# Kernel optimization log

Measured on AMD Instinct MI355X. Metric: run time of the kernel, lower is better.

## Reference

```python
import math
import jax, jax.numpy as jnp
import numpy as np


def setup_inputs() -> dict:
    key = jax.random.key(0)
    k1, k2, k3, k4 = jax.random.split(key, 4)
    B, CK, CV, T, H, W = 4, 64, 512, 8, 30, 30
    mk = jax.random.normal(k1, (B, CK, T, H, W), dtype=jnp.float32)
    qk = jax.random.normal(k2, (B, CK, H, W), dtype=jnp.float32)
    mv = jax.random.normal(k3, (B, CV, T, H, W), dtype=jnp.float32)
    qv = jax.random.normal(k4, (B, CV, H, W), dtype=jnp.float32)
    return {"mk": mk, "qk": qk, "mv": mv, "qv": qv}


def reference(mk, qk, mv, qv):
    # mk: [B, CK, T, H, W], qk: [B, CK, H, W]
    # mv: [B, CV, T, H, W], qv: [B, CV, H, W]
    B, CK, T, H, W = mk.shape
    CV = mv.shape[1]
    mkf = mk.reshape(B, CK, T * H * W)          # [B, CK, THW]
    qkf = qk.reshape(B, CK, H * W)              # [B, CK, HW]
    # distance-based affinity: (2 a.b - |a|^2) / sqrt(CK)
    a_sq = jnp.sum(mkf * mkf, axis=1)[:, :, None]        # [B, THW, 1]
    ab = jnp.einsum('bcm,bcq->bmq', mkf, qkf)            # [B, THW, HW]
    affinity = (2.0 * ab - a_sq) * (1.0 / math.sqrt(CK))
    # softmax over the memory dimension (THW)
    affinity = jax.nn.softmax(affinity, axis=1)          # [B, THW, HW]
    # value readout
    mvf = mv.reshape(B, CV, T * H * W)                   # [B, CV, THW]
    mem = jnp.einsum('bcm,bmq->bcq', mvf, affinity)      # [B, CV, HW]
    mem = mem.reshape(B, CV, H, W)
    return jnp.concatenate([mem, qv], axis=1)            # [B, 2*CV, H, W]
```

## Files before the change

kernel.cpp:

```cpp
#include <hip/hip_runtime.h>

#define B_ 4
#define CK 64
#define CV 512
#define HW_ 900
#define THW 7200
#define MT 96
#define QB 64
#define CVB 128
#define NS 3
#define MSPL (THW / NS)
#define NIT (MSPL / MT)
#define MVP (MT + 8)
#define MKP (CK + 8)

typedef __attribute__((ext_vector_type(4))) float f32x4;
typedef __attribute__((ext_vector_type(4))) float float4_;
typedef __attribute__((ext_vector_type(8))) short s16x8;
typedef __attribute__((ext_vector_type(4))) short s16x4;

__device__ __forceinline__ short f2bf(float f) {
  union { float f; unsigned u; } x; x.f = f;
  unsigned u = x.u;
  return (short)((u + 0x7fffu + ((u >> 16) & 1u)) >> 16);
}

#define NBLK_A 113
#define NBLK_B 900
#define NBLK_C 14400
#define NBLK_D 1800
__global__ __launch_bounds__(256) void prep_kernel(const float* __restrict__ mk,
                                                   const float* __restrict__ qk,
                                                   const float* __restrict__ mv,
                                                   const float* __restrict__ qv,
                                                   short* __restrict__ mkT,
                                                   short* __restrict__ qkb,
                                                   short* __restrict__ mvb,
                                                   float* __restrict__ asq,
                                                   float* __restrict__ out) {
  int bid = blockIdx.x;
  if (bid < NBLK_A) {
    int idx = bid * 256 + threadIdx.x;
    if (idx >= B_ * THW) return;
    int b = idx / THW, m = idx - b * THW;
    const float* src = mk + (size_t)b * CK * THW + m;
    short row[CK];
    float acc = 0.f;
#pragma unroll
    for (int k = 0; k < CK; ++k) {
      float v = src[(size_t)k * THW];
      acc += v * v;
      row[k] = f2bf(v);
    }
    short* dst = mkT + (size_t)idx * CK;
#pragma unroll
    for (int c = 0; c < CK / 8; ++c)
      *reinterpret_cast<s16x8*>(dst + c * 8) = *reinterpret_cast<s16x8*>(row + c * 8);
    asq[idx] = acc * 0.18033688011112042f;
  } else if (bid < NBLK_A + NBLK_B) {
    int i = (bid - NBLK_A) * 256 + threadIdx.x;
    if (i < B_ * CK * HW_) qkb[i] = f2bf(qk[i] * 0.36067376022224085f);
  } else if (bid < NBLK_A + NBLK_B + NBLK_C) {
    int i = (bid - (NBLK_A + NBLK_B)) * 256 + threadIdx.x;
    float4_ v = reinterpret_cast<const float4_*>(mv)[i];
    s16x4 o;
    o[0] = f2bf(v[0]); o[1] = f2bf(v[1]); o[2] = f2bf(v[2]); o[3] = f2bf(v[3]);
    *reinterpret_cast<s16x4*>(mvb + (size_t)i * 4) = o;
  } else {
    int i = (bid - (NBLK_A + NBLK_B + NBLK_C)) * 256 + threadIdx.x;
    const int perb = CV * HW_ / 4;
    int b = i / perb, r = i - b * perb;
    float4_ v = reinterpret_cast<const float4_*>(qv)[i];
    *reinterpret_cast<float4_*>(out + (size_t)b * 2 * CV * HW_ + CV * HW_ + (size_t)r * 4) = v;
  }
}

__global__ __launch_bounds__(256, 3) void attn_kernel(const short* __restrict__ mkT,
                                                      const short* __restrict__ qkb,
                                                      const short* __restrict__ mvb,
                                                      const float* __restrict__ asq,
                                                      float* __restrict__ part,
                                                      float* __restrict__ denomp) {
  __shared__ short mv_t[CVB][MVP];
  __shared__ short mk_t[MT][MKP];
  __shared__ short e_t[4][16][MVP];
  __shared__ float asq_t[MT];

  const int tid = threadIdx.x;
  const int wave = tid >> 6, lane = tid & 63;
  const int g = lane >> 4, c = lane & 15;
  const int qb = blockIdx.x;
  const int cvc = blockIdx.y & 3, s = blockIdx.y >> 2;
  const int b = blockIdx.z;
  const int q = qb * QB + wave * 16 + c;
  const int cv0 = cvc * CVB;

  s16x8 qf[2];
  {
    const short* qs = qkb + (size_t)b * CK * HW_;
#pragma unroll
    for (int ks = 0; ks < 2; ++ks)
#pragma unroll
      for (int j = 0; j < 8; ++j)
        qf[ks][j] = (q < HW_) ? qs[(size_t)(ks * 32 + g * 8 + j) * HW_ + q] : (short)0;
  }

  f32x4 acc[8];
#pragma unroll
  for (int i = 0; i < 8; ++i) acc[i] = (f32x4){0.f, 0.f, 0.f, 0.f};
  float denom = 0.f;

  const short* mksrc = mkT + (size_t)b * THW * CK;
  const short* mvsrc = mvb + ((size_t)b * CV + cv0) * THW;
  const float* asrc = asq + (size_t)b * THW;

  for (int it = 0; it < NIT; ++it) {
    const int m0 = s * MSPL + it * MT;
    {
      const short* s0 = mksrc + (size_t)m0 * CK;
#pragma unroll
      for (int p = 0; p < 3; ++p) {
        int ch = tid + p * 256;
        int r = ch >> 3, c8 = (ch & 7) * 8;
        *reinterpret_cast<s16x8*>(&mk_t[r][c8]) =
            *reinterpret_cast<const s16x8*>(s0 + r * CK + c8);
      }
#pragma unroll
      for (int p = 0; p < 6; ++p) {
        int ch = tid + p * 256;
        int r = ch / 12, c8 = (ch % 12) * 8;
        *reinterpret_cast<s16x8*>(&mv_t[r][c8]) =
            *reinterpret_cast<const s16x8*>(mvsrc + (size_t)r * THW + m0 + c8);
      }
      if (tid < MT) asq_t[tid] = asrc[m0 + tid];
    }
    __syncthreads();

#pragma unroll
    for (int mf = 0; mf < 6; ++mf) {
      f32x4 sa = (f32x4){0.f, 0.f, 0.f, 0.f};
#pragma unroll
      for (int ks = 0; ks < 2; ++ks) {
        s16x8 a = *reinterpret_cast<const s16x8*>(&mk_t[mf * 16 + c][ks * 32 + g * 8]);
        sa = __builtin_amdgcn_mfma_f32_16x16x32_bf16(a, qf[ks], sa, 0, 0, 0);
      }
      const int mb = mf * 16 + g * 4;
      s16x4 e4;
#pragma unroll
      for (int r = 0; r < 4; ++r) {
        float e = exp2f(sa[r] - asq_t[mb + r]);
        denom += e;
        e4[r] = f2bf(e);
      }
      *reinterpret_cast<s16x4*>(&e_t[wave][c][mb]) = e4;
    }

#pragma unroll
    for (int ks = 0; ks < 3; ++ks) {
      s16x8 bfr = *reinterpret_cast<const s16x8*>(&e_t[wave][c][ks * 32 + g * 8]);
#pragma unroll
      for (int cf = 0; cf < 8; ++cf) {
        s16x8 afr = *reinterpret_cast<const s16x8*>(&mv_t[cf * 16 + c][ks * 32 + g * 8]);
        acc[cf] = __builtin_amdgcn_mfma_f32_16x16x32_bf16(afr, bfr, acc[cf], 0, 0, 0);
      }
    }
    __syncthreads();
  }

  denom += __shfl_xor(denom, 16);
  denom += __shfl_xor(denom, 32);
  if (cvc == 0 && lane < 16)
    denomp[((size_t)s * B_ + b) * 960 + qb * QB + wave * 16 + lane] = denom;

  float* pb = part + (size_t)(((s * B_ + b) * 4 + cvc) * 15 + qb) * 8192 + wave * 16 + c;
#pragma unroll
  for (int cf = 0; cf < 8; ++cf)
#pragma unroll
    for (int r = 0; r < 4; ++r)
      pb[(size_t)(cf * 16 + g * 4 + r) * 64] = acc[cf][r];
}

__global__ __launch_bounds__(256) void finalize_kernel(const float* __restrict__ part,
                                                       const float* __restrict__ denomp,
                                                       float* __restrict__ out) {
  int t = blockIdx.x * 256 + threadIdx.x;
  int q4 = t & 15;
  int cvl = (t >> 4) & 127;
  int r1 = t >> 11;
  int qb = r1 % 15;
  int r2 = r1 / 15;
  int cvc = r2 & 3;
  int b = r2 >> 2;
  int q0 = qb * QB + q4 * 4;
  if (q0 >= HW_) return;
  const size_t sstr = (size_t)B_ * 4 * 15 * 8192;
  size_t base = (size_t)((b * 4 + cvc) * 15 + qb) * 8192 + cvl * 64 + q4 * 4;
  f32x4 p = *reinterpret_cast<const f32x4*>(part + base);
  f32x4 p1 = *reinterpret_cast<const f32x4*>(part + base + sstr);
  f32x4 p2 = *reinterpret_cast<const f32x4*>(part + base + 2 * sstr);
  p = p + p1 + p2;
  const float* dp = denomp + (size_t)b * 960 + q0;
  f32x4 d = *reinterpret_cast<const f32x4*>(dp) +
            *reinterpret_cast<const f32x4*>(dp + B_ * 960) +
            *reinterpret_cast<const f32x4*>(dp + 2 * B_ * 960);
  f32x4 o;
#pragma unroll
  for (int j = 0; j < 4; ++j) o[j] = p[j] / d[j];
  *reinterpret_cast<f32x4*>(out + (size_t)b * 2 * CV * HW_ +
                            (size_t)(cvc * CVB + cvl) * HW_ + q0) = o;
}

extern "C" void kernel_launch(void* const* d_in, const int* in_sizes, int n_in,
                              void* d_out, int out_size, void* d_ws, size_t ws_size,
                              hipStream_t stream) {
  const float* mk = (const float*)d_in[0];
  const float* qk = (const float*)d_in[1];
  const float* mv = (const float*)d_in[2];
  const float* qv = (const float*)d_in[3];
  float* out = (float*)d_out;

  char* ws = (char*)d_ws;
  short* mvb   = (short*)ws;
  short* mkT   = (short*)(ws + 29491200);
  short* qkb   = (short*)(ws + 33177600);
  float* asq   = (float*)(ws + 33638400);
  float* denomp= (float*)(ws + 33753600);
  float* part  = (float*)(ws + 33799680);

  prep_kernel<<<dim3(NBLK_A + NBLK_B + NBLK_C + NBLK_D), dim3(256), 0, stream>>>(
      mk, qk, mv, qv, mkT, qkb, mvb, asq, out);
  attn_kernel<<<dim3(15, 4 * NS, B_), dim3(256), 0, stream>>>(mkT, qkb, mvb, asq, part, denomp);
  finalize_kernel<<<dim3(1920), dim3(256), 0, stream>>>(part, denomp, out);
}
```

Baseline: 237.2 us.

## Load mk/mv fragments directly from global and share exp tile across waves

Removes the LDS staging of the mk and mv tiles. Each wave now reads its mk and mv MFMA fragments straight from global memory, and only the exp (affinity) tile goes through shared memory. The work is repartitioned so each wave owns 32 value channels across all 64 queries instead of 16 queries across all 128 channels. The change also truncates instead of rounding when converting to bf16 and raises the occupancy hint to 4 blocks. In exchange it relies on L1/L2 for the repeated mk reads, since every wave now loads the same mk rows, and it adds a small precision loss from truncation.

```diff
diff --git a/kernel.cpp b/kernel.cpp
--- a/kernel.cpp
+++ b/kernel.cpp
@@ -11,8 +11,7 @@
 #define NS 3
 #define MSPL (THW / NS)
 #define NIT (MSPL / MT)
-#define MVP (MT + 8)
-#define MKP (CK + 8)
+#define ETP 104
 
 typedef __attribute__((ext_vector_type(4))) float f32x4;
 typedef __attribute__((ext_vector_type(4))) float float4_;
@@ -75,16 +74,13 @@
   }
 }
 
-__global__ __launch_bounds__(256, 3) void attn_kernel(const short* __restrict__ mkT,
+__global__ __launch_bounds__(256, 4) void attn_kernel(const short* __restrict__ mkT,
                                                       const short* __restrict__ qkb,
                                                       const short* __restrict__ mvb,
                                                       const float* __restrict__ asq,
                                                       float* __restrict__ part,
                                                       float* __restrict__ denomp) {
-  __shared__ short mv_t[CVB][MVP];
-  __shared__ short mk_t[MT][MKP];
-  __shared__ short e_t[4][16][MVP];
-  __shared__ float asq_t[MT];
+  __shared__ short e_t[64][ETP];
 
   const int tid = threadIdx.x;
   const int wave = tid >> 6, lane = tid & 63;
@@ -93,76 +89,73 @@
   const int cvc = blockIdx.y & 3, s = blockIdx.y >> 2;
   const int b = blockIdx.z;
   const int q = qb * QB + wave * 16 + c;
-  const int cv0 = cvc * CVB;
-
-  s16x8 qf[2];
+
+  s16x8 qkf[2];
   {
     const short* qs = qkb + (size_t)b * CK * HW_;
 #pragma unroll
     for (int ks = 0; ks < 2; ++ks)
 #pragma unroll
       for (int j = 0; j < 8; ++j)
-        qf[ks][j] = (q < HW_) ? qs[(size_t)(ks * 32 + g * 8 + j) * HW_ + q] : (short)0;
+        qkf[ks][j] = (q < HW_) ? qs[(size_t)(ks * 32 + g * 8 + j) * HW_ + q] : (short)0;
   }
 
-  f32x4 acc[8];
-#pragma unroll
-  for (int i = 0; i < 8; ++i) acc[i] = (f32x4){0.f, 0.f, 0.f, 0.f};
+  f32x4 acc[2][4];
+#pragma unroll
+  for (int i = 0; i < 2; ++i)
+#pragma unroll
+    for (int j = 0; j < 4; ++j) acc[i][j] = (f32x4){0.f, 0.f, 0.f, 0.f};
   float denom = 0.f;
 
-  const short* mksrc = mkT + (size_t)b * THW * CK;
-  const short* mvsrc = mvb + ((size_t)b * CV + cv0) * THW;
-  const float* asrc = asq + (size_t)b * THW;
+  const short* mkb = mkT + (size_t)b * THW * CK;
+  const short* mvB = mvb + ((size_t)b * CV + cvc * CVB + wave * 32) * THW;
+  const float* asb = asq + (size_t)b * THW;
 
   for (int it = 0; it < NIT; ++it) {
     const int m0 = s * MSPL + it * MT;
-    {
-      const short* s0 = mksrc + (size_t)m0 * CK;
-#pragma unroll
-      for (int p = 0; p < 3; ++p) {
-        int ch = tid + p * 256;
-        int r = ch >> 3, c8 = (ch & 7) * 8;
-        *reinterpret_cast<s16x8*>(&mk_t[r][c8]) =
-            *reinterpret_cast<const s16x8*>(s0 + r * CK + c8);
+
+    s16x8 mvf[2][3];
+#pragma unroll
+    for (int af = 0; af < 2; ++af)
+#pragma unroll
+      for (int ks = 0; ks < 3; ++ks)
+        mvf[af][ks] = *reinterpret_cast<const s16x8*>(
+            mvB + (size_t)(af * 16 + c) * THW + m0 + ks * 32 + g * 8);
+
+#pragma unroll
+    for (int mf = 0; mf < 6; ++mf) {
+      f32x4 sa = (f32x4){0.f, 0.f, 0.f, 0.f};
+#pragma unroll
+      for (int ks = 0; ks < 2; ++ks) {
+        s16x8 a = *reinterpret_cast<const s16x8*>(
+            mkb + (size_t)(m0 + mf * 16 + c) * CK + ks * 32 + g * 8);
+        sa = __builtin_amdgcn_mfma_f32_16x16x32_bf16(a, qkf[ks], sa, 0, 0, 0);
       }
-#pragma unroll
-      for (int p = 0; p < 6; ++p) {
-        int ch = tid + p * 256;
-        int r = ch / 12, c8 = (ch % 12) * 8;
-        *reinterpret_cast<s16x8*>(&mv_t[r][c8]) =
-            *reinterpret_cast<const s16x8*>(mvsrc + (size_t)r * THW + m0 + c8);
+      f32x4 av = *reinterpret_cast<const f32x4*>(asb + m0 + mf * 16 + g * 4);
+      s16x4 e4;
+#pragma unroll
+      for (int r = 0; r < 4; ++r) {
+        float e = exp2f(sa[r] - av[r]);
+        denom += e;
+        union { float f; unsigned u; } cu; cu.f = e;
+        e4[r] = (short)(cu.u >> 16);
       }
-      if (tid < MT) asq_t[tid] = asrc[m0 + tid];
+      *reinterpret_cast<s16x4*>(&e_t[wave * 16 + c][mf * 16 + g * 4]) = e4;
     }
     __syncthreads();
 
 #pragma unroll
-    for (int mf = 0; mf < 6; ++mf) {
-      f32x4 sa = (f32x4){0.f, 0.f, 0.f, 0.f};
-#pragma unroll
-      for (int ks = 0; ks < 2; ++ks) {
-        s16x8 a = *reinterpret_cast<const s16x8*>(&mk_t[mf * 16 + c][ks * 32 + g * 8]);
-        sa = __builtin_amdgcn_mfma_f32_16x16x32_bf16(a, qf[ks], sa, 0, 0, 0);
-      }
-      const int mb = mf * 16 + g * 4;
-      s16x4 e4;
-#pragma unroll
-      for (int r = 0; r < 4; ++r) {
-        float e = exp2f(sa[r] - asq_t[mb + r]);
-        denom += e;
-        e4[r] = f2bf(e);
-      }
-      *reinterpret_cast<s16x4*>(&e_t[wave][c][mb]) = e4;
-    }
-
-#pragma unroll
     for (int ks = 0; ks < 3; ++ks) {
-      s16x8 bfr = *reinterpret_cast<const s16x8*>(&e_t[wave][c][ks * 32 + g * 8]);
-#pragma unroll
-      for (int cf = 0; cf < 8; ++cf) {
-        s16x8 afr = *reinterpret_cast<const s16x8*>(&mv_t[cf * 16 + c][ks * 32 + g * 8]);
-        acc[cf] = __builtin_amdgcn_mfma_f32_16x16x32_bf16(afr, bfr, acc[cf], 0, 0, 0);
-      }
+      s16x8 ef[4];
+#pragma unroll
+      for (int qf = 0; qf < 4; ++qf)
+        ef[qf] = *reinterpret_cast<const s16x8*>(&e_t[qf * 16 + c][ks * 32 + g * 8]);
+#pragma unroll
+      for (int af = 0; af < 2; ++af)
+#pragma unroll
+        for (int qf = 0; qf < 4; ++qf)
+          acc[af][qf] =
+              __builtin_amdgcn_mfma_f32_16x16x32_bf16(mvf[af][ks], ef[qf], acc[af][qf], 0, 0, 0);
     }
     __syncthreads();
   }
@@ -172,12 +165,14 @@
   if (cvc == 0 && lane < 16)
     denomp[((size_t)s * B_ + b) * 960 + qb * QB + wave * 16 + lane] = denom;
 
-  float* pb = part + (size_t)(((s * B_ + b) * 4 + cvc) * 15 + qb) * 8192 + wave * 16 + c;
-#pragma unroll
-  for (int cf = 0; cf < 8; ++cf)
-#pragma unroll
-    for (int r = 0; r < 4; ++r)
-      pb[(size_t)(cf * 16 + g * 4 + r) * 64] = acc[cf][r];
+  float* pb = part + (size_t)(((s * B_ + b) * 4 + cvc) * 15 + qb) * 8192;
+#pragma unroll
+  for (int af = 0; af < 2; ++af)
+#pragma unroll
+    for (int qf = 0; qf < 4; ++qf)
+#pragma unroll
+      for (int r = 0; r < 4; ++r)
+        pb[(size_t)(wave * 32 + af * 16 + g * 4 + r) * 64 + qf * 16 + c] = acc[af][qf][r];
 }
 
 __global__ __launch_bounds__(256) void finalize_kernel(const float* __restrict__ part,
```

New measurement: 284.6 us. 1.2x slower.
